# Optimization experiments

Measured on AMD Instinct MI355X. Metric: run time of the kernel, lower is better.

The kernel has to match this reference:

```python
import jax, jax.numpy as jnp
import numpy as np

HEAD_SIZE = 16
HIDDEN = 1024
NEG_INF = -1e9


def setup_inputs() -> dict:
    key = jax.random.key(0)
    ks = jax.random.split(key, 9)
    B, S, H = 2, 2048, HIDDEN
    q = jax.random.normal(ks[0], (B, S, H), dtype=jnp.float32)
    k = jax.random.normal(ks[1], (B, S, H), dtype=jnp.float32)
    v = jax.random.normal(ks[2], (B, S, H), dtype=jnp.float32)
    mask = jnp.ones((B, S), dtype=jnp.int32)
    scale = 1.0 / np.sqrt(H)
    wq = jax.random.normal(ks[3], (H, H), dtype=jnp.float32) * scale
    bq = jnp.zeros((H,), dtype=jnp.float32)
    wk = jax.random.normal(ks[4], (H, H), dtype=jnp.float32) * scale
    bk = jnp.zeros((H,), dtype=jnp.float32)
    wv = jax.random.normal(ks[5], (H, H), dtype=jnp.float32) * scale
    bv = jnp.zeros((H,), dtype=jnp.float32)
    return {"q": q, "k": k, "v": v, "mask": mask,
            "wq": wq, "bq": bq, "wk": wk, "bk": bk, "wv": wv, "bv": bv}


def _split_heads(x):
    # [B, S, H] -> [B, n_heads, S, head_dim]
    B, S, H = x.shape
    return x.reshape(B, S, HEAD_SIZE, H // HEAD_SIZE).transpose(0, 2, 1, 3)


def reference(q, k, v, mask, wq, bq, wk, bk, wv, bv):
    B, S, H = q.shape
    qh = _split_heads(q @ wq + bq)  # [B, nH, S, d]
    kh = _split_heads(k @ wk + bk)
    vh = _split_heads(v @ wv + bv)
    # scores scaled by sqrt(hidden_size) -- faithful to original (not head_dim)
    scores = jnp.einsum('bhqd,bhkd->bhqk', qh, kh) / jnp.sqrt(jnp.float32(H))
    # original: mask[0] of shape [B,S] -> [B,1,S,1], masks query rows
    m = mask.astype(jnp.float32)[:, None, :, None]  # [B,1,S,1]
    scores = scores + NEG_INF * (1.0 - m)
    weights = jax.nn.softmax(scores, axis=-1)
    out = jnp.einsum('bhqk,bhkd->bhqd', weights, vh)  # [B, nH, S, d]
    return out.transpose(0, 2, 1, 3).reshape(B, S, H)
```

## Files before the change

### kernel.cpp

```cpp
#include <hip/hip_runtime.h>
#include <hip/hip_bf16.h>
#include <math.h>

typedef __bf16 bf16_t;
typedef __bf16 bf16x8 __attribute__((ext_vector_type(8)));
typedef __bf16 bf16x4 __attribute__((ext_vector_type(4)));
typedef float floatx4 __attribute__((ext_vector_type(4)));

#define QSCALE 0.045084222f

__device__ __forceinline__ void gload_lds16(const bf16_t* g, bf16_t* l) {
  __builtin_amdgcn_global_load_lds(
      (const __attribute__((address_space(1))) void*)(g),
      (__attribute__((address_space(3))) void*)(l), 16, 0, 0);
}

__device__ __forceinline__ float fast_exp2(float x) {
  float r;
  asm("v_exp_f32 %0, %1" : "=v"(r) : "v"(x));
  return r;
}

__global__ __launch_bounds__(256) void prep_k(
    const float* __restrict__ q, const float* __restrict__ k,
    const float* __restrict__ v, const float* __restrict__ wq,
    const float* __restrict__ wk, const float* __restrict__ wv,
    bf16_t* __restrict__ xb, bf16_t* __restrict__ wt) {
  const int z = blockIdx.y;
  const int t = threadIdx.x;
  if (blockIdx.x < 2048) {
    const float* src = (z == 0) ? q : (z == 1) ? k : v;
    bf16_t* dst = xb + (size_t)z * 4194304u;
    const int i = (blockIdx.x * 256 + t) * 8;
    float4 f0 = *(const float4*)(src + i);
    float4 f1 = *(const float4*)(src + i + 4);
    bf16x8 hv;
    hv[0] = (bf16_t)f0.x; hv[1] = (bf16_t)f0.y;
    hv[2] = (bf16_t)f0.z; hv[3] = (bf16_t)f0.w;
    hv[4] = (bf16_t)f1.x; hv[5] = (bf16_t)f1.y;
    hv[6] = (bf16_t)f1.z; hv[7] = (bf16_t)f1.w;
    *(bf16x8*)(dst + i) = hv;
  } else {
    __shared__ float tile[32][33];
    const int bi = blockIdx.x - 2048;
    const int bx = bi & 31, by = bi >> 5;
    const float* src = (z == 0) ? wq : (z == 1) ? wk : wv;
    bf16_t* dst = wt + (size_t)z * 1048576u;
    const int tx = t & 31, ty = t >> 5;
    const int x = bx * 32 + tx, y = by * 32 + ty;
#pragma unroll
    for (int i = 0; i < 32; i += 8)
      tile[ty + i][tx] = src[(size_t)(y + i) * 1024 + x];
    __syncthreads();
    const int x2 = by * 32 + tx, y2 = bx * 32 + ty;
#pragma unroll
    for (int i = 0; i < 32; i += 8)
      dst[(size_t)(y2 + i) * 1024 + x2] = (bf16_t)tile[tx][ty + i];
  }
}

__global__ __launch_bounds__(256) void qkv_gemm_k(
    const bf16_t* __restrict__ xb3, const bf16_t* __restrict__ wt3,
    const float* __restrict__ bq, const float* __restrict__ bk,
    const float* __restrict__ bv, bf16_t* __restrict__ Qh,
    bf16_t* __restrict__ Kh, bf16_t* __restrict__ Vt) {
  const int proj = blockIdx.z;
  const bf16_t* X = xb3 + (size_t)proj * 4194304u;
  const bf16_t* Wt = wt3 + (size_t)proj * 1048576u;
  const float* bias = (proj == 0) ? bq : (proj == 1) ? bk : bv;

  __shared__ __align__(16) bf16_t As[128 * 64];
  __shared__ __align__(16) bf16_t Bs[128 * 64];

  const int t = threadIdx.x;
  const int lane = t & 63;
  const int w = t >> 6;
  const int wm = (w >> 1) * 64;
  const int wn = (w & 1) * 64;
  const int m0 = blockIdx.x * 128;
  const int n0 = blockIdx.y * 128;
  const int lm = lane & 15;
  const int lq = lane >> 4;

  int srow[4], sg[4];
#pragma unroll
  for (int c = 0; c < 4; ++c) {
    const int E = c * 2048 + t * 8;
    srow[c] = E >> 6;
    sg[c] = (((E >> 3) & 7) ^ (srow[c] & 7)) * 8;
  }

  floatx4 acc[4][4];
#pragma unroll
  for (int i = 0; i < 4; ++i)
#pragma unroll
    for (int j = 0; j < 4; ++j) acc[i][j] = (floatx4){0.f, 0.f, 0.f, 0.f};

  for (int k0 = 0; k0 < 1024; k0 += 64) {
    __syncthreads();
#pragma unroll
    for (int c = 0; c < 4; ++c) {
      const int E = c * 2048 + t * 8;
      gload_lds16(X + (size_t)(m0 + srow[c]) * 1024 + k0 + sg[c], As + E);
      gload_lds16(Wt + (size_t)(n0 + srow[c]) * 1024 + k0 + sg[c], Bs + E);
    }
    __syncthreads();

#pragma unroll
    for (int kc = 0; kc < 2; ++kc) {
      bf16x8 a[4], b[4];
#pragma unroll
      for (int i = 0; i < 4; ++i) {
        const int ch = ((kc * 4 + lq) ^ (lm & 7)) * 8;
        a[i] = *(const bf16x8*)(As + (wm + i * 16 + lm) * 64 + ch);
        b[i] = *(const bf16x8*)(Bs + (wn + i * 16 + lm) * 64 + ch);
      }
      if (proj < 2) {
#pragma unroll
        for (int i = 0; i < 4; ++i)
#pragma unroll
          for (int j = 0; j < 4; ++j)
            acc[i][j] = __builtin_amdgcn_mfma_f32_16x16x32_bf16(b[j], a[i],
                                                               acc[i][j], 0, 0, 0);
      } else {
#pragma unroll
        for (int i = 0; i < 4; ++i)
#pragma unroll
          for (int j = 0; j < 4; ++j)
            acc[i][j] = __builtin_amdgcn_mfma_f32_16x16x32_bf16(a[i], b[j],
                                                               acc[i][j], 0, 0, 0);
      }
    }
  }

  if (proj == 2) {
#pragma unroll
    for (int j = 0; j < 4; ++j) {
      const int gn = n0 + wn + j * 16 + lm;
      const float bval = bias[gn];
      const int h = gn >> 6, d = gn & 63;
#pragma unroll
      for (int i = 0; i < 4; ++i) {
        const int gm = m0 + wm + i * 16 + lq * 4;
        const int bb = gm >> 11, s0 = gm & 2047;
        bf16x4 pk;
#pragma unroll
        for (int ii = 0; ii < 4; ++ii) pk[ii] = (bf16_t)(acc[i][j][ii] + bval);
        *(bf16x4*)(Vt + (((size_t)bb * 16 + h) * 64 + d) * 2048 + s0) = pk;
      }
    }
  } else {
    bf16_t* outp = (proj == 0) ? Qh : Kh;
    const float scale = (proj == 0) ? QSCALE : 1.0f;
#pragma unroll
    for (int j = 0; j < 4; ++j) {
      const int nb = n0 + wn + j * 16 + lq * 4;
      float bs4[4];
#pragma unroll
      for (int ii = 0; ii < 4; ++ii) bs4[ii] = bias[nb + ii];
      const int h = nb >> 6, d0 = nb & 63;
#pragma unroll
      for (int i = 0; i < 4; ++i) {
        const int gm = m0 + wm + i * 16 + lm;
        const int bb = gm >> 11, s = gm & 2047;
        bf16x4 pk;
#pragma unroll
        for (int ii = 0; ii < 4; ++ii)
          pk[ii] = (bf16_t)((acc[i][j][ii] + bs4[ii]) * scale);
        *(bf16x4*)(outp + (((size_t)bb * 16 + h) * 2048 + s) * 64 + d0) = pk;
      }
    }
  }
}

__global__ __launch_bounds__(256) void attn_k(
    const bf16_t* __restrict__ Qh, const bf16_t* __restrict__ Kh,
    const bf16_t* __restrict__ Vt, float* __restrict__ out) {
  __shared__ __align__(16) bf16_t Ks[128 * 64];
  __shared__ __align__(16) bf16_t Vs[64 * 128];
  __shared__ __align__(16) bf16_t Ps[4][32 * 128];

  const int t = threadIdx.x;
  const int lane = t & 63;
  const int w = t >> 6;
  const int lm = lane & 15;
  const int lq = lane >> 4;
  const int b = blockIdx.x >> 4, h = blockIdx.x & 15;
  const int q0 = blockIdx.y * 128;
  const size_t bh = (size_t)b * 16 + h;
  const bf16_t* Qb = Qh + bh * (2048 * 64);
  const bf16_t* Kb = Kh + bh * (2048 * 64);
  const bf16_t* Vb = Vt + bh * (64 * 2048);

  bf16x8 qf[2][2];
#pragma unroll
  for (int im = 0; im < 2; ++im)
#pragma unroll
    for (int kc = 0; kc < 2; ++kc)
      qf[im][kc] = *(const bf16x8*)(Qb +
          (size_t)(q0 + w * 32 + im * 16 + lm) * 64 + kc * 32 + lq * 8);

  bf16x8 ones;
#pragma unroll
  for (int j = 0; j < 8; ++j) ones[j] = (bf16_t)1.0f;

  floatx4 accO[2][4], accL[2];
#pragma unroll
  for (int im = 0; im < 2; ++im) {
#pragma unroll
    for (int jd = 0; jd < 4; ++jd) accO[im][jd] = (floatx4){0.f, 0.f, 0.f, 0.f};
    accL[im] = (floatx4){0.f, 0.f, 0.f, 0.f};
  }

  bf16x8 kv[8];

#define LOAD_KV(kt)                                                          \
  {                                                                          \
    _Pragma("unroll") for (int c = 0; c < 4; ++c) {                          \
      const int e = c * 2048 + t * 8;                                        \
      const int key = e >> 6, gk = ((e >> 3) & 7) ^ (key & 7);               \
      kv[c] = *(const bf16x8*)(Kb + (size_t)((kt) + key) * 64 + gk * 8);     \
      const int vr = e >> 7, gv = ((e >> 3) & 15) ^ (vr & 15);               \
      kv[4 + c] = *(const bf16x8*)(Vb + (size_t)vr * 2048 + (kt) + gv * 8);  \
    }                                                                        \
  }

  LOAD_KV(0);

  for (int kt = 0; kt < 2048; kt += 128) {
    __syncthreads();
#pragma unroll
    for (int c = 0; c < 4; ++c) {
      const int e = c * 2048 + t * 8;
      *(bf16x8*)(Ks + e) = kv[c];
      *(bf16x8*)(Vs + e) = kv[4 + c];
    }
    __syncthreads();

    if (kt + 128 < 2048) LOAD_KV(kt + 128);

    floatx4 accS[2][8];
#pragma unroll
    for (int jn = 0; jn < 8; ++jn) {
      const int krow = jn * 16 + lm;
      const bf16x8 k0 = *(const bf16x8*)(Ks + krow * 64 + ((lq) ^ (lm & 7)) * 8);
      const bf16x8 k1 = *(const bf16x8*)(Ks + krow * 64 + ((4 + lq) ^ (lm & 7)) * 8);
#pragma unroll
      for (int im = 0; im < 2; ++im) {
        floatx4 z = {0.f, 0.f, 0.f, 0.f};
        z = __builtin_amdgcn_mfma_f32_16x16x32_bf16(k0, qf[im][0], z, 0, 0, 0);
        z = __builtin_amdgcn_mfma_f32_16x16x32_bf16(k1, qf[im][1], z, 0, 0, 0);
        accS[im][jn] = z;
      }
    }

#pragma unroll
    for (int im = 0; im < 2; ++im) {
      const int pr = im * 16 + lm;
#pragma unroll
      for (int jn = 0; jn < 8; ++jn) {
        bf16x4 pk;
#pragma unroll
        for (int ii = 0; ii < 4; ++ii) pk[ii] = (bf16_t)fast_exp2(accS[im][jn][ii]);
        const int c2 = ((jn * 2) + (lq >> 1)) ^ lm;
        *(bf16x4*)(Ps[w] + pr * 128 + c2 * 8 + (lq & 1) * 4) = pk;
      }
    }
    asm volatile("s_waitcnt lgkmcnt(0)" ::: "memory");

#pragma unroll
    for (int kc = 0; kc < 4; ++kc) {
      bf16x8 ap[2];
#pragma unroll
      for (int im = 0; im < 2; ++im)
        ap[im] = *(const bf16x8*)(Ps[w] + (im * 16 + lm) * 128 +
                                  ((kc * 4 + lq) ^ lm) * 8);
#pragma unroll
      for (int jd = 0; jd < 4; ++jd) {
        const bf16x8 vf = *(const bf16x8*)(Vs + (jd * 16 + lm) * 128 +
                                           ((kc * 4 + lq) ^ lm) * 8);
#pragma unroll
        for (int im = 0; im < 2; ++im)
          accO[im][jd] =
              __builtin_amdgcn_mfma_f32_16x16x32_bf16(vf, ap[im], accO[im][jd], 0, 0, 0);
      }
#pragma unroll
      for (int im = 0; im < 2; ++im)
        accL[im] = __builtin_amdgcn_mfma_f32_16x16x32_bf16(ones, ap[im],
                                                           accL[im], 0, 0, 0);
    }
  }
#undef LOAD_KV

  float inv[2];
#pragma unroll
  for (int im = 0; im < 2; ++im) inv[im] = 1.0f / accL[im][0];

#pragma unroll
  for (int im = 0; im < 2; ++im) {
    const int s = q0 + w * 32 + im * 16 + lm;
    float* op = out + ((size_t)b * 2048 + s) * 1024 + h * 64 + lq * 4;
#pragma unroll
    for (int jd = 0; jd < 4; ++jd) {
      float4 o;
      o.x = accO[im][jd][0] * inv[im];
      o.y = accO[im][jd][1] * inv[im];
      o.z = accO[im][jd][2] * inv[im];
      o.w = accO[im][jd][3] * inv[im];
      *(float4*)(op + jd * 16) = o;
    }
  }
}

extern "C" void kernel_launch(void* const* d_in, const int* in_sizes, int n_in,
                              void* d_out, int out_size, void* d_ws, size_t ws_size,
                              hipStream_t stream) {
  (void)in_sizes; (void)n_in; (void)out_size; (void)ws_size;
  const float* q = (const float*)d_in[0];
  const float* k = (const float*)d_in[1];
  const float* v = (const float*)d_in[2];
  const float* wq = (const float*)d_in[4];
  const float* bq = (const float*)d_in[5];
  const float* wk = (const float*)d_in[6];
  const float* bk = (const float*)d_in[7];
  const float* wv = (const float*)d_in[8];
  const float* bv = (const float*)d_in[9];
  float* out = (float*)d_out;

  bf16_t* ws = (bf16_t*)d_ws;
  bf16_t* Xb = ws;
  bf16_t* Wt = ws + 12582912u;
  bf16_t* Qh = Wt + 3145728u;
  bf16_t* Kh = Qh + 4194304u;
  bf16_t* Vt = Kh + 4194304u;

  prep_k<<<dim3(3072, 3, 1), dim3(256, 1, 1), 0, stream>>>(
      q, k, v, wq, wk, wv, Xb, Wt);
  qkv_gemm_k<<<dim3(32, 8, 3), dim3(256, 1, 1), 0, stream>>>(
      Xb, Wt, bq, bk, bv, Qh, Kh, Vt);
  attn_k<<<dim3(32, 16, 1), dim3(256, 1, 1), 0, stream>>>(Qh, Kh, Vt, out);
}
```

Measured before the change: 196.8 us.

## Shrink attention tiles to 64 queries and 64 keys for higher occupancy

Reworks the attention kernel so each block handles 64 queries with 16 per wave, and iterates over keys in 64-key chunks instead of 128. LDS use and registers drop, which allows more waves per CU and doubles the grid to 1024 blocks. It also raises wave priority around the MFMA sections. The cost is twice as many K/V loads per query, less reuse of each loaded K/V tile, and more barriers per key sweep.

```diff
diff --git a/kernel.cpp b/kernel.cpp
--- a/kernel.cpp
+++ b/kernel.cpp
@@ -173,12 +173,12 @@
   }
 }
 
-__global__ __launch_bounds__(256) void attn_k(
+__global__ __launch_bounds__(256, 4) void attn_k(
     const bf16_t* __restrict__ Qh, const bf16_t* __restrict__ Kh,
     const bf16_t* __restrict__ Vt, float* __restrict__ out) {
-  __shared__ __align__(16) bf16_t Ks[128 * 64];
-  __shared__ __align__(16) bf16_t Vs[64 * 128];
-  __shared__ __align__(16) bf16_t Ps[4][32 * 128];
+  __shared__ __align__(16) bf16_t Ks[64 * 64];
+  __shared__ __align__(16) bf16_t Vs[64 * 64];
+  __shared__ __align__(16) bf16_t Ps[4][16 * 64];
 
   const int t = threadIdx.x;
   const int lane = t & 63;
@@ -186,129 +186,107 @@
   const int lm = lane & 15;
   const int lq = lane >> 4;
   const int b = blockIdx.x >> 4, h = blockIdx.x & 15;
-  const int q0 = blockIdx.y * 128;
+  const int q0 = blockIdx.y * 64;
   const size_t bh = (size_t)b * 16 + h;
   const bf16_t* Qb = Qh + bh * (2048 * 64);
   const bf16_t* Kb = Kh + bh * (2048 * 64);
   const bf16_t* Vb = Vt + bh * (64 * 2048);
 
-  bf16x8 qf[2][2];
-#pragma unroll
-  for (int im = 0; im < 2; ++im)
-#pragma unroll
-    for (int kc = 0; kc < 2; ++kc)
-      qf[im][kc] = *(const bf16x8*)(Qb +
-          (size_t)(q0 + w * 32 + im * 16 + lm) * 64 + kc * 32 + lq * 8);
+  bf16x8 qf[2];
+#pragma unroll
+  for (int kc = 0; kc < 2; ++kc)
+    qf[kc] = *(const bf16x8*)(Qb +
+        (size_t)(q0 + w * 16 + lm) * 64 + kc * 32 + lq * 8);
 
   bf16x8 ones;
 #pragma unroll
   for (int j = 0; j < 8; ++j) ones[j] = (bf16_t)1.0f;
 
-  floatx4 accO[2][4], accL[2];
-#pragma unroll
-  for (int im = 0; im < 2; ++im) {
-#pragma unroll
-    for (int jd = 0; jd < 4; ++jd) accO[im][jd] = (floatx4){0.f, 0.f, 0.f, 0.f};
-    accL[im] = (floatx4){0.f, 0.f, 0.f, 0.f};
-  }
-
-  bf16x8 kv[8];
+  floatx4 accO[4], accL;
+#pragma unroll
+  for (int jd = 0; jd < 4; ++jd) accO[jd] = (floatx4){0.f, 0.f, 0.f, 0.f};
+  accL = (floatx4){0.f, 0.f, 0.f, 0.f};
+
+  bf16x8 kv[4];
 
 #define LOAD_KV(kt)                                                          \
   {                                                                          \
-    _Pragma("unroll") for (int c = 0; c < 4; ++c) {                          \
+    _Pragma("unroll") for (int c = 0; c < 2; ++c) {                          \
       const int e = c * 2048 + t * 8;                                        \
       const int key = e >> 6, gk = ((e >> 3) & 7) ^ (key & 7);               \
       kv[c] = *(const bf16x8*)(Kb + (size_t)((kt) + key) * 64 + gk * 8);     \
-      const int vr = e >> 7, gv = ((e >> 3) & 15) ^ (vr & 15);               \
-      kv[4 + c] = *(const bf16x8*)(Vb + (size_t)vr * 2048 + (kt) + gv * 8);  \
+      kv[2 + c] = *(const bf16x8*)(Vb + (size_t)key * 2048 + (kt) + gk * 8); \
     }                                                                        \
   }
 
   LOAD_KV(0);
 
-  for (int kt = 0; kt < 2048; kt += 128) {
-    __syncthreads();
-#pragma unroll
-    for (int c = 0; c < 4; ++c) {
+  for (int kt = 0; kt < 2048; kt += 64) {
+    __syncthreads();
+#pragma unroll
+    for (int c = 0; c < 2; ++c) {
       const int e = c * 2048 + t * 8;
       *(bf16x8*)(Ks + e) = kv[c];
-      *(bf16x8*)(Vs + e) = kv[4 + c];
-    }
-    __syncthreads();
-
-    if (kt + 128 < 2048) LOAD_KV(kt + 128);
-
-    floatx4 accS[2][8];
-#pragma unroll
-    for (int jn = 0; jn < 8; ++jn) {
+      *(bf16x8*)(Vs + e) = kv[2 + c];
+    }
+    __syncthreads();
+
+    if (kt + 64 < 2048) LOAD_KV(kt + 64);
+
+    floatx4 accS[4];
+    __builtin_amdgcn_s_setprio(1);
+#pragma unroll
+    for (int jn = 0; jn < 4; ++jn) {
       const int krow = jn * 16 + lm;
       const bf16x8 k0 = *(const bf16x8*)(Ks + krow * 64 + ((lq) ^ (lm & 7)) * 8);
       const bf16x8 k1 = *(const bf16x8*)(Ks + krow * 64 + ((4 + lq) ^ (lm & 7)) * 8);
-#pragma unroll
-      for (int im = 0; im < 2; ++im) {
-        floatx4 z = {0.f, 0.f, 0.f, 0.f};
-        z = __builtin_amdgcn_mfma_f32_16x16x32_bf16(k0, qf[im][0], z, 0, 0, 0);
-        z = __builtin_amdgcn_mfma_f32_16x16x32_bf16(k1, qf[im][1], z, 0, 0, 0);
-        accS[im][jn] = z;
-      }
-    }
-
-#pragma unroll
-    for (int im = 0; im < 2; ++im) {
-      const int pr = im * 16 + lm;
-#pragma unroll
-      for (int jn = 0; jn < 8; ++jn) {
-        bf16x4 pk;
-#pragma unroll
-        for (int ii = 0; ii < 4; ++ii) pk[ii] = (bf16_t)fast_exp2(accS[im][jn][ii]);
-        const int c2 = ((jn * 2) + (lq >> 1)) ^ lm;
-        *(bf16x4*)(Ps[w] + pr * 128 + c2 * 8 + (lq & 1) * 4) = pk;
-      }
+      floatx4 z = {0.f, 0.f, 0.f, 0.f};
+      z = __builtin_amdgcn_mfma_f32_16x16x32_bf16(k0, qf[0], z, 0, 0, 0);
+      z = __builtin_amdgcn_mfma_f32_16x16x32_bf16(k1, qf[1], z, 0, 0, 0);
+      accS[jn] = z;
+    }
+    __builtin_amdgcn_s_setprio(0);
+
+#pragma unroll
+    for (int jn = 0; jn < 4; ++jn) {
+      bf16x4 pk;
+#pragma unroll
+      for (int ii = 0; ii < 4; ++ii) pk[ii] = (bf16_t)fast_exp2(accS[jn][ii]);
+      const int c2 = (jn * 2 + (lq >> 1)) ^ (lm & 7);
+      *(bf16x4*)(Ps[w] + lm * 64 + c2 * 8 + (lq & 1) * 4) = pk;
     }
     asm volatile("s_waitcnt lgkmcnt(0)" ::: "memory");
 
-#pragma unroll
-    for (int kc = 0; kc < 4; ++kc) {
-      bf16x8 ap[2];
-#pragma unroll
-      for (int im = 0; im < 2; ++im)
-        ap[im] = *(const bf16x8*)(Ps[w] + (im * 16 + lm) * 128 +
-                                  ((kc * 4 + lq) ^ lm) * 8);
+    __builtin_amdgcn_s_setprio(1);
+#pragma unroll
+    for (int kc = 0; kc < 2; ++kc) {
+      const bf16x8 ap = *(const bf16x8*)(Ps[w] + lm * 64 +
+                                         ((kc * 4 + lq) ^ (lm & 7)) * 8);
 #pragma unroll
       for (int jd = 0; jd < 4; ++jd) {
-        const bf16x8 vf = *(const bf16x8*)(Vs + (jd * 16 + lm) * 128 +
-                                           ((kc * 4 + lq) ^ lm) * 8);
-#pragma unroll
-        for (int im = 0; im < 2; ++im)
-          accO[im][jd] =
-              __builtin_amdgcn_mfma_f32_16x16x32_bf16(vf, ap[im], accO[im][jd], 0, 0, 0);
-      }
-#pragma unroll
-      for (int im = 0; im < 2; ++im)
-        accL[im] = __builtin_amdgcn_mfma_f32_16x16x32_bf16(ones, ap[im],
-                                                           accL[im], 0, 0, 0);
-    }
+        const bf16x8 vf = *(const bf16x8*)(Vs + (jd * 16 + lm) * 64 +
+                                           ((kc * 4 + lq) ^ (lm & 7)) * 8);
+        accO[jd] =
+            __builtin_amdgcn_mfma_f32_16x16x32_bf16(vf, ap, accO[jd], 0, 0, 0);
+      }
+      accL = __builtin_amdgcn_mfma_f32_16x16x32_bf16(ones, ap, accL, 0, 0, 0);
+    }
+    __builtin_amdgcn_s_setprio(0);
   }
 #undef LOAD_KV
 
-  float inv[2];
-#pragma unroll
-  for (int im = 0; im < 2; ++im) inv[im] = 1.0f / accL[im][0];
-
-#pragma unroll
-  for (int im = 0; im < 2; ++im) {
-    const int s = q0 + w * 32 + im * 16 + lm;
-    float* op = out + ((size_t)b * 2048 + s) * 1024 + h * 64 + lq * 4;
-#pragma unroll
-    for (int jd = 0; jd < 4; ++jd) {
-      float4 o;
-      o.x = accO[im][jd][0] * inv[im];
-      o.y = accO[im][jd][1] * inv[im];
-      o.z = accO[im][jd][2] * inv[im];
-      o.w = accO[im][jd][3] * inv[im];
-      *(float4*)(op + jd * 16) = o;
-    }
+  const float inv = 1.0f / accL[0];
+
+  const int s = q0 + w * 16 + lm;
+  float* op = out + ((size_t)b * 2048 + s) * 1024 + h * 64 + lq * 4;
+#pragma unroll
+  for (int jd = 0; jd < 4; ++jd) {
+    float4 o;
+    o.x = accO[jd][0] * inv;
+    o.y = accO[jd][1] * inv;
+    o.z = accO[jd][2] * inv;
+    o.w = accO[jd][3] * inv;
+    *(float4*)(op + jd * 16) = o;
   }
 }
 
@@ -338,5 +316,5 @@
       q, k, v, wq, wk, wv, Xb, Wt);
   qkv_gemm_k<<<dim3(32, 8, 3), dim3(256, 1, 1), 0, stream>>>(
       Xb, Wt, bq, bk, bv, Qh, Kh, Vt);
-  attn_k<<<dim3(32, 16, 1), dim3(256, 1, 1), 0, stream>>>(Qh, Kh, Vt, out);
-}
+  attn_k<<<dim3(32, 32, 1), dim3(256, 1, 1), 0, stream>>>(Qh, Kh, Vt, out);
+}
```

After: 202.6 us. 1.03x slower.
